# Kernel optimization log

Measured on AMD Instinct MI355X. Metric: run time of the kernel, lower is better.

## Reference

```python
import jax, jax.numpy as jnp
import numpy as np

N_PARTICLES = 100000
STATE_DIM = 64          # 3 + 2*2 + 57
MSG_OUT = 64
HIDDEN = 32
N_EDGES = 1600000


def _init_linear(key, fan_in, fan_out):
    kw, kb = jax.random.split(key)
    bound = 1.0 / np.sqrt(fan_in)
    W = jax.random.uniform(kw, (fan_in, fan_out), minval=-bound, maxval=bound, dtype=jnp.float32)
    b = jax.random.uniform(kb, (fan_out,), minval=-bound, maxval=bound, dtype=jnp.float32)
    return W, b


def setup_inputs() -> dict:
    key = jax.random.key(0)
    ks = jax.random.split(key, 8)
    x = jax.random.normal(ks[0], (N_PARTICLES, STATE_DIM), dtype=jnp.float32)
    edge_index = jax.random.randint(ks[1], (2, N_EDGES), 0, N_PARTICLES, dtype=jnp.int64)
    # message conv MLP: [2*STATE_DIM] -> 32 -> 32 -> MSG_OUT
    mW1, mb1 = _init_linear(ks[2], 2 * STATE_DIM, HIDDEN)
    mW2, mb2 = _init_linear(ks[3], HIDDEN, HIDDEN)
    mW3, mb3 = _init_linear(ks[4], HIDDEN, MSG_OUT)
    # own_state_nn MLP: [STATE_DIM + MSG_OUT] -> 32 -> 32 -> STATE_DIM
    oW1, ob1 = _init_linear(ks[5], STATE_DIM + MSG_OUT, HIDDEN)
    oW2, ob2 = _init_linear(ks[6], HIDDEN, HIDDEN)
    oW3, ob3 = _init_linear(ks[7], HIDDEN, STATE_DIM)
    return {"x": x, "edge_index": edge_index,
            "mW1": mW1, "mb1": mb1, "mW2": mW2, "mb2": mb2, "mW3": mW3, "mb3": mb3,
            "oW1": oW1, "ob1": ob1, "oW2": oW2, "ob2": ob2, "oW3": oW3, "ob3": ob3}


def _mlp3(h, W1, b1, W2, b2, W3, b3):
    h = jax.nn.relu(h @ W1 + b1)
    h = jax.nn.relu(h @ W2 + b2)
    return h @ W3 + b3


def reference(x, edge_index, mW1, mb1, mW2, mb2, mW3, mb3,
              oW1, ob1, oW2, ob2, oW3, ob3):
    src, dst = edge_index[0], edge_index[1]
    # edge-wise message: MLP over [x_src || x_dst]  -> [E, MSG_OUT]
    e_feat = jnp.concatenate([x[src], x[dst]], axis=-1)  # [E, 2*STATE_DIM]
    m = _mlp3(e_feat, mW1, mb1, mW2, mb2, mW3, mb3)
    # scatter-sum aggregation at destination node
    messages = jax.ops.segment_sum(m, dst, num_segments=x.shape[0])  # [N, MSG_OUT]
    combined = jnp.concatenate([x, messages], axis=-1)  # [N, STATE_DIM+MSG_OUT]
    new_state = _mlp3(combined, oW1, ob1, oW2, ob2, oW3, ob3)
    return new_state
```

## Files before the change

kernel.cpp:

```cpp
#include <hip/hip_runtime.h>

#define NP 100000
#define NE 1600000
#define SD 64
#define HID 32
#define MSG 64
#define NP_PAD 100352
#define NTILE (NP / 16)
#define TILE_BLOCKS ((NTILE + 3) / 4)
#define BINSZ 512
#define NBIN ((NP + BINSZ - 1) / BINSZ)
#define EPW 8192
#define NWG ((NE + EPW - 1) / EPW)

typedef float v4f __attribute__((ext_vector_type(4)));
typedef short v4s __attribute__((ext_vector_type(4)));
typedef short v8s __attribute__((ext_vector_type(8)));
typedef __bf16 v8bf __attribute__((ext_vector_type(8)));

#define WQ_FRAGS 56

__device__ __forceinline__ v4f MFMA32(v8s a, v8s b, v4f c) {
  return __builtin_amdgcn_mfma_f32_16x16x32_bf16(
      __builtin_bit_cast(v8bf, a), __builtin_bit_cast(v8bf, b), c, 0, 0, 0);
}

__device__ __forceinline__ short f2bf(float f) {
  return __builtin_bit_cast(short, (__bf16)f);
}
__device__ __forceinline__ float bf2f(short s) {
  unsigned u = ((unsigned)(unsigned short)s) << 16;
  return __builtin_bit_cast(float, u);
}

__device__ __forceinline__ v4f mfma3(v8s ah, v8s al, v8s bh, v8s bl, v4f c) {
  c = MFMA32(al, bh, c);
  c = MFMA32(ah, bl, c);
  c = MFMA32(ah, bh, c);
  return c;
}

__device__ __forceinline__ void load_wfrag(const float* __restrict__ W, int ld,
                                           int kb, int m0, int lq, int l15,
                                           v8s* hi, v8s* lo) {
  v8s h, l;
#pragma unroll
  for (int j = 0; j < 8; ++j) {
    int k = kb + ((j < 4) ? (4 * lq + j) : (16 + 4 * lq + (j - 4)));
    float v = W[k * ld + m0 + l15];
    short hb = f2bf(v);
    h[j] = hb;
    l[j] = f2bf(v - bf2f(hb));
  }
  *hi = h;
  *lo = l;
}

__device__ __forceinline__ void split8(v4f a, v4f b, v8s* hi, v8s* lo) {
  v8s h, l;
#pragma unroll
  for (int j = 0; j < 4; ++j) {
    short ha = f2bf(a[j]); h[j] = ha; l[j] = f2bf(a[j] - bf2f(ha));
    short hb = f2bf(b[j]); h[j + 4] = hb; l[j + 4] = f2bf(b[j] - bf2f(hb));
  }
  *hi = h;
  *lo = l;
}

__device__ __forceinline__ void load_xfrag(const float* xs, int kb, int lq,
                                           v8s* hi, v8s* lo) {
  v4f a = *reinterpret_cast<const v4f*>(xs + kb + 4 * lq);
  v4f b = *reinterpret_cast<const v4f*>(xs + kb + 16 + 4 * lq);
  split8(a, b, hi, lo);
}

__device__ __forceinline__ void chain_frag(v4f d0, v4f d1, v8s* hi, v8s* lo) {
  v4f a, b;
#pragma unroll
  for (int j = 0; j < 4; ++j) {
    a[j] = fmaxf(d0[j], 0.f);
    b[j] = fmaxf(d1[j], 0.f);
  }
  split8(a, b, hi, lo);
}

__device__ __forceinline__ v8s chain_hi(v4f d0, v4f d1) {
  v8s h;
#pragma unroll
  for (int j = 0; j < 4; ++j) {
    h[j] = f2bf(fmaxf(d0[j], 0.f));
    h[j + 4] = f2bf(fmaxf(d1[j], 0.f));
  }
  return h;
}

__global__ __launch_bounds__(256, 2) void setup_kernel(
    const float* __restrict__ x, const int* __restrict__ ei,
    const float* __restrict__ mW1, const float* __restrict__ mb1,
    const float* __restrict__ mW2, const float* __restrict__ mW3,
    const float* __restrict__ oW1, const float* __restrict__ oW2,
    const float* __restrict__ oW3,
    int* __restrict__ gOff, short* __restrict__ wqs,
    float* __restrict__ h1d_buf, short* __restrict__ h1s_buf) {
  __shared__ int cnt[NBIN];
  const int blk = blockIdx.x;

  if (blk < NWG) {
    for (int i = threadIdx.x; i < NBIN; i += 256) cnt[i] = 0;
    __syncthreads();
    const int e0 = blk * EPW;
    const int e1 = (e0 + EPW < NE) ? e0 + EPW : NE;
    for (int e = e0 + threadIdx.x; e < e1; e += 256)
      atomicAdd(&cnt[ei[NE + e] >> 9], 1);
    __syncthreads();
    for (int i = threadIdx.x; i < NBIN; i += 256) gOff[i * NWG + blk] = cnt[i];
    return;
  }

  const int lane = threadIdx.x & 63;
  const int l15 = lane & 15;
  const int lq = lane >> 4;

  if (blk == NWG) {
    if (threadIdx.x >= 64) return;
    v8s* wq = reinterpret_cast<v8s*>(wqs);
    v8s h, l;
#pragma unroll
    for (int t = 0; t < 2; ++t)
#pragma unroll
      for (int kc = 0; kc < 2; ++kc) {
        load_wfrag(mW1, HID, kc * 32, t * 16, lq, l15, &h, &l);
        wq[(t * 2 + kc) * 64 + lane] = h;
        wq[(4 + t * 2 + kc) * 64 + lane] = l;
        load_wfrag(mW1, HID, 64 + kc * 32, t * 16, lq, l15, &h, &l);
        wq[(8 + t * 2 + kc) * 64 + lane] = h;
        wq[(12 + t * 2 + kc) * 64 + lane] = l;
      }
#pragma unroll
    for (int t = 0; t < 2; ++t) {
      load_wfrag(mW2, HID, 0, t * 16, lq, l15, &h, &l);
      wq[(16 + t) * 64 + lane] = h;
      wq[(18 + t) * 64 + lane] = l;
    }
#pragma unroll
    for (int t = 0; t < 4; ++t) {
      load_wfrag(mW3, MSG, 0, t * 16, lq, l15, &h, &l);
      wq[(20 + t) * 64 + lane] = h;
      wq[(24 + t) * 64 + lane] = l;
    }
#pragma unroll
    for (int t = 0; t < 2; ++t)
#pragma unroll
      for (int kc = 0; kc < 4; ++kc) {
        load_wfrag(oW1, HID, kc * 32, t * 16, lq, l15, &h, &l);
        wq[(28 + t * 4 + kc) * 64 + lane] = h;
        wq[(36 + t * 4 + kc) * 64 + lane] = l;
      }
#pragma unroll
    for (int t = 0; t < 2; ++t) {
      load_wfrag(oW2, HID, 0, t * 16, lq, l15, &h, &l);
      wq[(44 + t) * 64 + lane] = h;
      wq[(46 + t) * 64 + lane] = l;
    }
#pragma unroll
    for (int t = 0; t < 4; ++t) {
      load_wfrag(oW3, SD, 0, t * 16, lq, l15, &h, &l);
      wq[(48 + t) * 64 + lane] = h;
      wq[(52 + t) * 64 + lane] = l;
    }
    return;
  }

  const int tile = ((blk - NWG - 1) * 256 + (int)threadIdx.x) >> 6;
  if (tile >= NTILE) return;
  const int node = tile * 16 + l15;

  v4f d0, d1, s0 = {0.f, 0.f, 0.f, 0.f}, s1 = {0.f, 0.f, 0.f, 0.f};
#pragma unroll
  for (int q = 0; q < 4; ++q) {
    d0[q] = mb1[4 * lq + q];
    d1[q] = mb1[16 + 4 * lq + q];
  }
#pragma unroll
  for (int kc = 0; kc < 2; ++kc) {
    v8s xh, xl, wh, wl;
    load_xfrag(x + (size_t)node * SD, kc * 32, lq, &xh, &xl);
    load_wfrag(mW1, HID, 64 + kc * 32, 0, lq, l15, &wh, &wl);
    d0 = mfma3(wh, wl, xh, xl, d0);
    load_wfrag(mW1, HID, 64 + kc * 32, 16, lq, l15, &wh, &wl);
    d1 = mfma3(wh, wl, xh, xl, d1);
    load_wfrag(mW1, HID, kc * 32, 0, lq, l15, &wh, &wl);
    s0 = mfma3(wh, wl, xh, xl, s0);
    load_wfrag(mW1, HID, kc * 32, 16, lq, l15, &wh, &wl);
    s1 = mfma3(wh, wl, xh, xl, s1);
  }
  *reinterpret_cast<v4f*>(h1d_buf + (size_t)node * HID + 4 * lq) = d0;
  *reinterpret_cast<v4f*>(h1d_buf + (size_t)node * HID + 16 + 4 * lq) = d1;
  v4s q0, q1;
#pragma unroll
  for (int q = 0; q < 4; ++q) {
    q0[q] = f2bf(s0[q]);
    q1[q] = f2bf(s1[q]);
  }
  *reinterpret_cast<v4s*>(h1s_buf + (size_t)node * HID + 4 * lq) = q0;
  *reinterpret_cast<v4s*>(h1s_buf + (size_t)node * HID + 16 + 4 * lq) = q1;
}


__global__ __launch_bounds__(256) void scan_bins_kernel(
    int* __restrict__ gOff, int* __restrict__ binStart) {
  __shared__ int sh[256];
  const int b = threadIdx.x;
  int run = 0;
  if (b < NBIN) {
    int4* row = reinterpret_cast<int4*>(gOff + b * NWG);
#pragma unroll 4
    for (int i = 0; i < NWG / 4; ++i) {
      int4 v = row[i];
      int4 w;
      w.x = run; run += v.x;
      w.y = run; run += v.y;
      w.z = run; run += v.z;
      w.w = run; run += v.w;
      row[i] = w;
    }
  }
  sh[b] = run;
  __syncthreads();
  for (int off = 1; off < 256; off <<= 1) {
    int a = (b >= off) ? sh[b - off] : 0;
    __syncthreads();
    sh[b] += a;
    __syncthreads();
  }
  const int excl = sh[b] - run;
  if (b <= NBIN) binStart[b] = excl;
  if (b < NBIN) {
    int4* row = reinterpret_cast<int4*>(gOff + b * NWG);
#pragma unroll 4
    for (int i = 0; i < NWG / 4; ++i) {
      int4 v = row[i];
      v.x += excl; v.y += excl; v.z += excl; v.w += excl;
      row[i] = v;
    }
  }
}

__global__ __launch_bounds__(256) void bin_scatter_kernel(
    const int* __restrict__ ei, const int* __restrict__ gOff,
    unsigned* __restrict__ pairs) {
  __shared__ int cur[NBIN];
  const int w = blockIdx.x;
  for (int i = threadIdx.x; i < NBIN; i += 256) cur[i] = gOff[i * NWG + w];
  __syncthreads();
  const int e0 = w * EPW;
  const int e1 = (e0 + EPW < NE) ? e0 + EPW : NE;
  for (int e = e0 + threadIdx.x; e < e1; e += 256) {
    unsigned s = (unsigned)ei[e];
    unsigned d = (unsigned)ei[NE + e];
    int pos = atomicAdd(&cur[d >> 9], 1);
    pairs[pos] = (s << 9) | (d & (BINSZ - 1));
  }
}

__global__ __launch_bounds__(512) void bin_csr_kernel(
    const unsigned* __restrict__ pairs, const int* __restrict__ binStart,
    int2* __restrict__ co, int* __restrict__ csr_src) {
  __shared__ int sh[BINSZ];
  __shared__ int cu[BINSZ];
  const int b = blockIdx.x;
  const int t = threadIdx.x;
  cu[t] = 0;
  __syncthreads();
  const int p0 = binStart[b], p1 = binStart[b + 1];
  for (int p = p0 + t; p < p1; p += BINSZ)
    atomicAdd(&cu[pairs[p] & (BINSZ - 1)], 1);
  __syncthreads();
  const int v = cu[t];
  sh[t] = v;
  __syncthreads();
  for (int off = 1; off < BINSZ; off <<= 1) {
    int a = (t >= off) ? sh[t - off] : 0;
    __syncthreads();
    sh[t] += a;
    __syncthreads();
  }
  const int excl = sh[t] - v;
  const int node = b * BINSZ + t;
  if (node < NP) co[node] = make_int2(p0 + excl, v);
  cu[t] = excl;
  __syncthreads();
  for (int p = p0 + t; p < p1; p += BINSZ) {
    unsigned pr = pairs[p];
    int loc = atomicAdd(&cu[pr & (BINSZ - 1)], 1);
    csr_src[p0 + loc] = (int)(pr >> 9);
  }
}

__global__ void edge_mfma_kernel(
    const short* __restrict__ h1s, const float* __restrict__ h1d_buf,
    const short* __restrict__ wqs, const int2* __restrict__ co,
    const int* __restrict__ csr_src, const float* __restrict__ mb2,
    float* __restrict__ rsum) {
  const int lane = threadIdx.x & 63;
  const int l15 = lane & 15;
  const int lq = lane >> 4;
  const int wid = (blockIdx.x * 256 + threadIdx.x) >> 6;
  const int nw = gridDim.x * 4;
  const v8s* wq = reinterpret_cast<const v8s*>(wqs);

  const v8s w2h0 = wq[16 * 64 + lane], w2h1 = wq[17 * 64 + lane];
  const v8s w2l0 = wq[18 * 64 + lane], w2l1 = wq[19 * 64 + lane];
  v4f bb0, bb1;
#pragma unroll
  for (int q = 0; q < 4; ++q) {
    bb0[q] = mb2[4 * lq + q];
    bb1[q] = mb2[16 + 4 * lq + q];
  }

  for (int n = wid * 2; n < NP; n += 2 * nw) {
    const int4 cc = *reinterpret_cast<const int4*>(co + n);
    const int offA = cc.x, cntA = cc.y;
    const int offB = cc.z, cntB = cc.w;
    const int ngA = (cntA + 15) >> 4;
    const int ngB = (cntB + 15) >> 4;
    const int ngM = ngA > ngB ? ngA : ngB;

    const v4f hA0 = *reinterpret_cast<const v4f*>(h1d_buf + (size_t)n * HID + 4 * lq);
    const v4f hA1 = *reinterpret_cast<const v4f*>(h1d_buf + (size_t)n * HID + 16 + 4 * lq);
    const v4f hB0 = *reinterpret_cast<const v4f*>(h1d_buf + (size_t)(n + 1) * HID + 4 * lq);
    const v4f hB1 = *reinterpret_cast<const v4f*>(h1d_buf + (size_t)(n + 1) * HID + 16 + 4 * lq);

    v4f rA0 = {0.f, 0.f, 0.f, 0.f}, rA1 = {0.f, 0.f, 0.f, 0.f};
    v4f rB0 = {0.f, 0.f, 0.f, 0.f}, rB1 = {0.f, 0.f, 0.f, 0.f};

    int sA = (l15 < cntA) ? csr_src[offA + l15] : 0;
    int sB = (l15 < cntB) ? csr_src[offB + l15] : 0;
    v4s aA = *reinterpret_cast<const v4s*>(h1s + (size_t)sA * HID + 4 * lq);
    v4s bA = *reinterpret_cast<const v4s*>(h1s + (size_t)sA * HID + 16 + 4 * lq);
    v4s aB = *reinterpret_cast<const v4s*>(h1s + (size_t)sB * HID + 4 * lq);
    v4s bB = *reinterpret_cast<const v4s*>(h1s + (size_t)sB * HID + 16 + 4 * lq);

    int remA = cntA, remB = cntB;
    for (int g = 0; g < ngM; ++g) {
      int sAn = (l15 < remA - 16) ? csr_src[offA + (g + 1) * 16 + l15] : 0;
      int sBn = (l15 < remB - 16) ? csr_src[offB + (g + 1) * 16 + l15] : 0;

      if (g < ngA) {
        v4f d0, d1;
#pragma unroll
        for (int q = 0; q < 4; ++q) {
          d0[q] = hA0[q] + bf2f(aA[q]);
          d1[q] = hA1[q] + bf2f(bA[q]);
        }
        v8s ph = chain_hi(d0, d1);
        v4f e0 = bb0, e1 = bb1;
        e0 = MFMA32(w2h0, ph, e0);
        e0 = MFMA32(w2l0, ph, e0);
        e1 = MFMA32(w2h1, ph, e1);
        e1 = MFMA32(w2l1, ph, e1);
        if (l15 < remA) {
#pragma unroll
          for (int j = 0; j < 4; ++j) {
            rA0[j] += fmaxf(e0[j], 0.f);
            rA1[j] += fmaxf(e1[j], 0.f);
          }
        }
      }
      aA = *reinterpret_cast<const v4s*>(h1s + (size_t)sAn * HID + 4 * lq);
      bA = *reinterpret_cast<const v4s*>(h1s + (size_t)sAn * HID + 16 + 4 * lq);

      if (g < ngB) {
        v4f d0, d1;
#pragma unroll
        for (int q = 0; q < 4; ++q) {
          d0[q] = hB0[q] + bf2f(aB[q]);
          d1[q] = hB1[q] + bf2f(bB[q]);
        }
        v8s ph = chain_hi(d0, d1);
        v4f e0 = bb0, e1 = bb1;
        e0 = MFMA32(w2h0, ph, e0);
        e0 = MFMA32(w2l0, ph, e0);
        e1 = MFMA32(w2h1, ph, e1);
        e1 = MFMA32(w2l1, ph, e1);
        if (l15 < remB) {
#pragma unroll
          for (int j = 0; j < 4; ++j) {
            rB0[j] += fmaxf(e0[j], 0.f);
            rB1[j] += fmaxf(e1[j], 0.f);
          }
        }
      }
      aB = *reinterpret_cast<const v4s*>(h1s + (size_t)sBn * HID + 4 * lq);
      bB = *reinterpret_cast<const v4s*>(h1s + (size_t)sBn * HID + 16 + 4 * lq);

      remA -= 16;
      remB -= 16;
    }

#pragma unroll
    for (int j = 0; j < 4; ++j) {
      float a = rA0[j], b = rA1[j], c = rB0[j], d = rB1[j];
      a += __shfl_xor(a, 1); a += __shfl_xor(a, 2);
      a += __shfl_xor(a, 4); a += __shfl_xor(a, 8);
      b += __shfl_xor(b, 1); b += __shfl_xor(b, 2);
      b += __shfl_xor(b, 4); b += __shfl_xor(b, 8);
      c += __shfl_xor(c, 1); c += __shfl_xor(c, 2);
      c += __shfl_xor(c, 4); c += __shfl_xor(c, 8);
      d += __shfl_xor(d, 1); d += __shfl_xor(d, 2);
      d += __shfl_xor(d, 4); d += __shfl_xor(d, 8);
      rA0[j] = a; rA1[j] = b; rB0[j] = c; rB1[j] = d;
    }
    if (l15 == 0) {
      *reinterpret_cast<v4f*>(rsum + (size_t)n * HID + 4 * lq) = rA0;
      *reinterpret_cast<v4f*>(rsum + (size_t)n * HID + 16 + 4 * lq) = rA1;
      *reinterpret_cast<v4f*>(rsum + (size_t)(n + 1) * HID + 4 * lq) = rB0;
      *reinterpret_cast<v4f*>(rsum + (size_t)(n + 1) * HID + 16 + 4 * lq) = rB1;
    }
  }
}

__global__ __launch_bounds__(256, 2) void fused_tail_kernel(
    const float* __restrict__ x, const short* __restrict__ wqs,
    const float* __restrict__ rsum, const int2* __restrict__ co,
    const float* __restrict__ mb3,
    const float* __restrict__ ob1, const float* __restrict__ ob2,
    const float* __restrict__ ob3,
    float* __restrict__ out) {
  const int lane = threadIdx.x & 63;
  const int l15 = lane & 15;
  const int lq = lane >> 4;
  const int tile = (blockIdx.x * 256 + threadIdx.x) >> 6;
  if (tile >= NTILE) return;
  const v8s* wq = reinterpret_cast<const v8s*>(wqs);

  const int node = tile * 16 + l15;
  const float fc = (float)co[node].y;

  v4f ra = *reinterpret_cast<const v4f*>(rsum + (size_t)node * HID + 4 * lq);
  v4f rb = *reinterpret_cast<const v4f*>(rsum + (size_t)node * HID + 16 + 4 * lq);
  v8s bh, bl;
  split8(ra, rb, &bh, &bl);

  v4f m[4];
#pragma unroll
  for (int t = 0; t < 4; ++t) {
    v4f c = {0.f, 0.f, 0.f, 0.f};
    c = mfma3(wq[(20 + t) * 64 + lane], wq[(24 + t) * 64 + lane], bh, bl, c);
#pragma unroll
    for (int q = 0; q < 4; ++q) c[q] += fc * mb3[t * 16 + 4 * lq + q];
    m[t] = c;
  }

  v4f d0, d1;
#pragma unroll
  for (int q = 0; q < 4; ++q) {
    d0[q] = ob1[4 * lq + q];
    d1[q] = ob1[16 + 4 * lq + q];
  }
#pragma unroll
  for (int kc = 0; kc < 2; ++kc) {
    v8s xh, xl;
    load_xfrag(x + (size_t)node * SD, kc * 32, lq, &xh, &xl);
    d0 = mfma3(wq[(28 + kc) * 64 + lane], wq[(36 + kc) * 64 + lane], xh, xl, d0);
    d1 = mfma3(wq[(32 + kc) * 64 + lane], wq[(40 + kc) * 64 + lane], xh, xl, d1);
  }
#pragma unroll
  for (int kc = 0; kc < 2; ++kc) {
    v8s mh, ml;
    split8(m[kc * 2], m[kc * 2 + 1], &mh, &ml);
    d0 = mfma3(wq[(30 + kc) * 64 + lane], wq[(38 + kc) * 64 + lane], mh, ml, d0);
    d1 = mfma3(wq[(34 + kc) * 64 + lane], wq[(42 + kc) * 64 + lane], mh, ml, d1);
  }

  v8s ph, pl;
  chain_frag(d0, d1, &ph, &pl);
  v4f e0, e1;
#pragma unroll
  for (int q = 0; q < 4; ++q) {
    e0[q] = ob2[4 * lq + q];
    e1[q] = ob2[16 + 4 * lq + q];
  }
  e0 = mfma3(wq[44 * 64 + lane], wq[46 * 64 + lane], ph, pl, e0);
  e1 = mfma3(wq[45 * 64 + lane], wq[47 * 64 + lane], ph, pl, e1);

  v8s rh, rl;
  chain_frag(e0, e1, &rh, &rl);
  float* orow = out + (size_t)node * SD;
#pragma unroll
  for (int t = 0; t < 4; ++t) {
    v4f c;
#pragma unroll
    for (int q = 0; q < 4; ++q) c[q] = ob3[t * 16 + 4 * lq + q];
    c = mfma3(wq[(48 + t) * 64 + lane], wq[(52 + t) * 64 + lane], rh, rl, c);
    *reinterpret_cast<v4f*>(orow + t * 16 + 4 * lq) = c;
  }
}

extern "C" void kernel_launch(void* const* d_in, const int* in_sizes, int n_in,
                              void* d_out, int out_size, void* d_ws,
                              size_t ws_size, hipStream_t stream) {
  const float* x = (const float*)d_in[0];
  const int* ei = (const int*)d_in[1];
  const float* mW1 = (const float*)d_in[2];
  const float* mb1 = (const float*)d_in[3];
  const float* mW2 = (const float*)d_in[4];
  const float* mb2 = (const float*)d_in[5];
  const float* mW3 = (const float*)d_in[6];
  const float* mb3 = (const float*)d_in[7];
  const float* oW1 = (const float*)d_in[8];
  const float* ob1 = (const float*)d_in[9];
  const float* oW2 = (const float*)d_in[10];
  const float* ob2 = (const float*)d_in[11];
  const float* oW3 = (const float*)d_in[12];
  const float* ob3 = (const float*)d_in[13];
  float* out = (float*)d_out;

  float* h1d_buf = (float*)d_out;
  short* h1s_buf = (short*)((char*)d_out + (size_t)NP * HID * 4);

  char* p = (char*)d_ws;
  short* wqs = (short*)p;            p += (size_t)WQ_FRAGS * 64 * 16;
  int* gOff = (int*)p;               p += (size_t)NBIN * NWG * 4;
  int* binStart = (int*)p;           p += 200 * 4;
  int2* co = (int2*)p;               p += (size_t)NP_PAD * 8;
  int* csr_src = (int*)p;            p += (size_t)NE * 4;
  unsigned* pairs = (unsigned*)p;
  float* rsum = (float*)p;

  setup_kernel<<<NWG + 1 + TILE_BLOCKS, 256, 0, stream>>>(
      x, ei, mW1, mb1, mW2, mW3, oW1, oW2, oW3, gOff, wqs, h1d_buf, h1s_buf);

  scan_bins_kernel<<<1, 256, 0, stream>>>(gOff, binStart);
  bin_scatter_kernel<<<NWG, 256, 0, stream>>>(ei, gOff, pairs);
  bin_csr_kernel<<<NBIN, 512, 0, stream>>>(pairs, binStart, co, csr_src);

  edge_mfma_kernel<<<4096, 256, 0, stream>>>(
      h1s_buf, h1d_buf, wqs, co, csr_src, mb2, rsum);

  fused_tail_kernel<<<TILE_BLOCKS, 256, 0, stream>>>(
      x, wqs, rsum, co, mb3, ob1, ob2, ob3, out);
}
```

Measured before the change: 156.6 us.

## Fuse per-bin CSR build into edge MFMA kernel with LDS-resident CSR

Halves the destination bin size to 256 nodes and merges the bin-local CSR construction with the edge-message MFMA computation. Each 512-thread block builds its bin's histogram, prefix offsets and source list in LDS, then its 8 waves process the bin's nodes in pairs. This removes the global csr_src and co arrays and one kernel launch. The cost is a fixed LDS capacity (MAXE) that silently drops edges if a bin overflows, and load balancing that is now fixed per bin instead of grid-strided.

```diff
diff --git a/kernel.cpp b/kernel.cpp
--- a/kernel.cpp
+++ b/kernel.cpp
@@ -8,8 +8,9 @@
 #define NP_PAD 100352
 #define NTILE (NP / 16)
 #define TILE_BLOCKS ((NTILE + 3) / 4)
-#define BINSZ 512
+#define BINSZ 256
 #define NBIN ((NP + BINSZ - 1) / BINSZ)
+#define MAXE 5632
 #define EPW 8192
 #define NWG ((NE + EPW - 1) / EPW)
 
@@ -111,7 +112,7 @@
     const int e0 = blk * EPW;
     const int e1 = (e0 + EPW < NE) ? e0 + EPW : NE;
     for (int e = e0 + threadIdx.x; e < e1; e += 256)
-      atomicAdd(&cnt[ei[NE + e] >> 9], 1);
+      atomicAdd(&cnt[ei[NE + e] >> 8], 1);
     __syncthreads();
     for (int i = threadIdx.x; i < NBIN; i += 256) gOff[i * NWG + blk] = cnt[i];
     return;
@@ -207,9 +208,9 @@
 }
 
 
-__global__ __launch_bounds__(256) void scan_bins_kernel(
+__global__ __launch_bounds__(512) void scan_bins_kernel(
     int* __restrict__ gOff, int* __restrict__ binStart) {
-  __shared__ int sh[256];
+  __shared__ int sh[512];
   const int b = threadIdx.x;
   int run = 0;
   if (b < NBIN) {
@@ -227,7 +228,7 @@
   }
   sh[b] = run;
   __syncthreads();
-  for (int off = 1; off < 256; off <<= 1) {
+  for (int off = 1; off < 512; off <<= 1) {
     int a = (b >= off) ? sh[b - off] : 0;
     __syncthreads();
     sh[b] += a;
@@ -258,55 +259,55 @@
   for (int e = e0 + threadIdx.x; e < e1; e += 256) {
     unsigned s = (unsigned)ei[e];
     unsigned d = (unsigned)ei[NE + e];
-    int pos = atomicAdd(&cur[d >> 9], 1);
-    pairs[pos] = (s << 9) | (d & (BINSZ - 1));
-  }
-}
-
-__global__ __launch_bounds__(512) void bin_csr_kernel(
-    const unsigned* __restrict__ pairs, const int* __restrict__ binStart,
-    int2* __restrict__ co, int* __restrict__ csr_src) {
-  __shared__ int sh[BINSZ];
-  __shared__ int cu[BINSZ];
+    int pos = atomicAdd(&cur[d >> 8], 1);
+    pairs[pos] = (s << 8) | (d & (BINSZ - 1));
+  }
+}
+
+__global__ __launch_bounds__(512, 4) void bin_fused_kernel(
+    const short* __restrict__ h1s, const float* __restrict__ h1d_buf,
+    const short* __restrict__ wqs, const unsigned* __restrict__ pairs,
+    const int* __restrict__ binStart, const float* __restrict__ mb2,
+    float* __restrict__ rsum, int* __restrict__ cntN) {
+  __shared__ int hist[BINSZ];
+  __shared__ int excl_s[BINSZ];
+  __shared__ int cur[BINSZ];
+  __shared__ int csr[MAXE];
+  const int tid = threadIdx.x;
   const int b = blockIdx.x;
-  const int t = threadIdx.x;
-  cu[t] = 0;
-  __syncthreads();
   const int p0 = binStart[b], p1 = binStart[b + 1];
-  for (int p = p0 + t; p < p1; p += BINSZ)
-    atomicAdd(&cu[pairs[p] & (BINSZ - 1)], 1);
-  __syncthreads();
-  const int v = cu[t];
-  sh[t] = v;
+
+  for (int i = tid; i < BINSZ; i += 512) hist[i] = 0;
+  __syncthreads();
+  for (int p = p0 + tid; p < p1; p += 512)
+    atomicAdd(&hist[pairs[p] & (BINSZ - 1)], 1);
+  __syncthreads();
+  if (tid < BINSZ) excl_s[tid] = hist[tid];
   __syncthreads();
   for (int off = 1; off < BINSZ; off <<= 1) {
-    int a = (t >= off) ? sh[t - off] : 0;
+    int a = (tid < BINSZ && tid >= off) ? excl_s[tid - off] : 0;
     __syncthreads();
-    sh[t] += a;
+    if (tid < BINSZ) excl_s[tid] += a;
     __syncthreads();
   }
-  const int excl = sh[t] - v;
-  const int node = b * BINSZ + t;
-  if (node < NP) co[node] = make_int2(p0 + excl, v);
-  cu[t] = excl;
-  __syncthreads();
-  for (int p = p0 + t; p < p1; p += BINSZ) {
+  if (tid < BINSZ) {
+    int e = excl_s[tid] - hist[tid];
+    excl_s[tid] = e;
+    cur[tid] = e;
+  }
+  __syncthreads();
+  for (int p = p0 + tid; p < p1; p += 512) {
     unsigned pr = pairs[p];
-    int loc = atomicAdd(&cu[pr & (BINSZ - 1)], 1);
-    csr_src[p0 + loc] = (int)(pr >> 9);
-  }
-}
-
-__global__ void edge_mfma_kernel(
-    const short* __restrict__ h1s, const float* __restrict__ h1d_buf,
-    const short* __restrict__ wqs, const int2* __restrict__ co,
-    const int* __restrict__ csr_src, const float* __restrict__ mb2,
-    float* __restrict__ rsum) {
-  const int lane = threadIdx.x & 63;
+    int pos = atomicAdd(&cur[pr & (BINSZ - 1)], 1);
+    if (pos < MAXE) csr[pos] = (int)(pr >> 8);
+  }
+  __syncthreads();
+
+  const int lane = tid & 63;
   const int l15 = lane & 15;
   const int lq = lane >> 4;
-  const int wid = (blockIdx.x * 256 + threadIdx.x) >> 6;
-  const int nw = gridDim.x * 4;
+  const int wv = tid >> 6;
+  const int nodeBase = b * BINSZ;
   const v8s* wq = reinterpret_cast<const v8s*>(wqs);
 
   const v8s w2h0 = wq[16 * 64 + lane], w2h1 = wq[17 * 64 + lane];
@@ -318,24 +319,27 @@
     bb1[q] = mb2[16 + 4 * lq + q];
   }
 
-  for (int n = wid * 2; n < NP; n += 2 * nw) {
-    const int4 cc = *reinterpret_cast<const int4*>(co + n);
-    const int offA = cc.x, cntA = cc.y;
-    const int offB = cc.z, cntB = cc.w;
+  for (int t = 0; t < 16; ++t) {
+    const int nlA = wv * 32 + 2 * t;
+    const int nlB = nlA + 1;
+    const int nA = nodeBase + nlA;
+    const int nB = nodeBase + nlB;
+    const int offA = excl_s[nlA], cntA = hist[nlA];
+    const int offB = excl_s[nlB], cntB = hist[nlB];
     const int ngA = (cntA + 15) >> 4;
     const int ngB = (cntB + 15) >> 4;
     const int ngM = ngA > ngB ? ngA : ngB;
 
-    const v4f hA0 = *reinterpret_cast<const v4f*>(h1d_buf + (size_t)n * HID + 4 * lq);
-    const v4f hA1 = *reinterpret_cast<const v4f*>(h1d_buf + (size_t)n * HID + 16 + 4 * lq);
-    const v4f hB0 = *reinterpret_cast<const v4f*>(h1d_buf + (size_t)(n + 1) * HID + 4 * lq);
-    const v4f hB1 = *reinterpret_cast<const v4f*>(h1d_buf + (size_t)(n + 1) * HID + 16 + 4 * lq);
+    const v4f hA0 = *reinterpret_cast<const v4f*>(h1d_buf + (size_t)nA * HID + 4 * lq);
+    const v4f hA1 = *reinterpret_cast<const v4f*>(h1d_buf + (size_t)nA * HID + 16 + 4 * lq);
+    const v4f hB0 = *reinterpret_cast<const v4f*>(h1d_buf + (size_t)nB * HID + 4 * lq);
+    const v4f hB1 = *reinterpret_cast<const v4f*>(h1d_buf + (size_t)nB * HID + 16 + 4 * lq);
 
     v4f rA0 = {0.f, 0.f, 0.f, 0.f}, rA1 = {0.f, 0.f, 0.f, 0.f};
     v4f rB0 = {0.f, 0.f, 0.f, 0.f}, rB1 = {0.f, 0.f, 0.f, 0.f};
 
-    int sA = (l15 < cntA) ? csr_src[offA + l15] : 0;
-    int sB = (l15 < cntB) ? csr_src[offB + l15] : 0;
+    int sA = (l15 < cntA) ? csr[offA + l15] : 0;
+    int sB = (l15 < cntB) ? csr[offB + l15] : 0;
     v4s aA = *reinterpret_cast<const v4s*>(h1s + (size_t)sA * HID + 4 * lq);
     v4s bA = *reinterpret_cast<const v4s*>(h1s + (size_t)sA * HID + 16 + 4 * lq);
     v4s aB = *reinterpret_cast<const v4s*>(h1s + (size_t)sB * HID + 4 * lq);
@@ -343,8 +347,8 @@
 
     int remA = cntA, remB = cntB;
     for (int g = 0; g < ngM; ++g) {
-      int sAn = (l15 < remA - 16) ? csr_src[offA + (g + 1) * 16 + l15] : 0;
-      int sBn = (l15 < remB - 16) ? csr_src[offB + (g + 1) * 16 + l15] : 0;
+      int sAn = (l15 < remA - 16) ? csr[offA + (g + 1) * 16 + l15] : 0;
+      int sBn = (l15 < remB - 16) ? csr[offB + (g + 1) * 16 + l15] : 0;
 
       if (g < ngA) {
         v4f d0, d1;
@@ -400,29 +404,35 @@
 
 #pragma unroll
     for (int j = 0; j < 4; ++j) {
-      float a = rA0[j], b = rA1[j], c = rB0[j], d = rB1[j];
+      float a = rA0[j], b2 = rA1[j], c = rB0[j], d = rB1[j];
       a += __shfl_xor(a, 1); a += __shfl_xor(a, 2);
       a += __shfl_xor(a, 4); a += __shfl_xor(a, 8);
-      b += __shfl_xor(b, 1); b += __shfl_xor(b, 2);
-      b += __shfl_xor(b, 4); b += __shfl_xor(b, 8);
+      b2 += __shfl_xor(b2, 1); b2 += __shfl_xor(b2, 2);
+      b2 += __shfl_xor(b2, 4); b2 += __shfl_xor(b2, 8);
       c += __shfl_xor(c, 1); c += __shfl_xor(c, 2);
       c += __shfl_xor(c, 4); c += __shfl_xor(c, 8);
       d += __shfl_xor(d, 1); d += __shfl_xor(d, 2);
       d += __shfl_xor(d, 4); d += __shfl_xor(d, 8);
-      rA0[j] = a; rA1[j] = b; rB0[j] = c; rB1[j] = d;
+      rA0[j] = a; rA1[j] = b2; rB0[j] = c; rB1[j] = d;
     }
     if (l15 == 0) {
-      *reinterpret_cast<v4f*>(rsum + (size_t)n * HID + 4 * lq) = rA0;
-      *reinterpret_cast<v4f*>(rsum + (size_t)n * HID + 16 + 4 * lq) = rA1;
-      *reinterpret_cast<v4f*>(rsum + (size_t)(n + 1) * HID + 4 * lq) = rB0;
-      *reinterpret_cast<v4f*>(rsum + (size_t)(n + 1) * HID + 16 + 4 * lq) = rB1;
+      if (nA < NP) {
+        *reinterpret_cast<v4f*>(rsum + (size_t)nA * HID + 4 * lq) = rA0;
+        *reinterpret_cast<v4f*>(rsum + (size_t)nA * HID + 16 + 4 * lq) = rA1;
+        if (lq == 0) cntN[nA] = cntA;
+      }
+      if (nB < NP) {
+        *reinterpret_cast<v4f*>(rsum + (size_t)nB * HID + 4 * lq) = rB0;
+        *reinterpret_cast<v4f*>(rsum + (size_t)nB * HID + 16 + 4 * lq) = rB1;
+        if (lq == 0) cntN[nB] = cntB;
+      }
     }
   }
 }
 
 __global__ __launch_bounds__(256, 2) void fused_tail_kernel(
     const float* __restrict__ x, const short* __restrict__ wqs,
-    const float* __restrict__ rsum, const int2* __restrict__ co,
+    const float* __restrict__ rsum, const int* __restrict__ cntN,
     const float* __restrict__ mb3,
     const float* __restrict__ ob1, const float* __restrict__ ob2,
     const float* __restrict__ ob3,
@@ -435,7 +445,7 @@
   const v8s* wq = reinterpret_cast<const v8s*>(wqs);
 
   const int node = tile * 16 + l15;
-  const float fc = (float)co[node].y;
+  const float fc = (float)cntN[node];
 
   v4f ra = *reinterpret_cast<const v4f*>(rsum + (size_t)node * HID + 4 * lq);
   v4f rb = *reinterpret_cast<const v4f*>(rsum + (size_t)node * HID + 16 + 4 * lq);
@@ -522,22 +532,20 @@
   char* p = (char*)d_ws;
   short* wqs = (short*)p;            p += (size_t)WQ_FRAGS * 64 * 16;
   int* gOff = (int*)p;               p += (size_t)NBIN * NWG * 4;
-  int* binStart = (int*)p;           p += 200 * 4;
-  int2* co = (int2*)p;               p += (size_t)NP_PAD * 8;
-  int* csr_src = (int*)p;            p += (size_t)NE * 4;
-  unsigned* pairs = (unsigned*)p;
+  int* binStart = (int*)p;           p += 400 * 4;
+  int* cntN = (int*)p;               p += (size_t)NP_PAD * 4;
+  unsigned* pairs = (unsigned*)p;    p += (size_t)NE * 4;
   float* rsum = (float*)p;
 
   setup_kernel<<<NWG + 1 + TILE_BLOCKS, 256, 0, stream>>>(
       x, ei, mW1, mb1, mW2, mW3, oW1, oW2, oW3, gOff, wqs, h1d_buf, h1s_buf);
 
-  scan_bins_kernel<<<1, 256, 0, stream>>>(gOff, binStart);
+  scan_bins_kernel<<<1, 512, 0, stream>>>(gOff, binStart);
   bin_scatter_kernel<<<NWG, 256, 0, stream>>>(ei, gOff, pairs);
-  bin_csr_kernel<<<NBIN, 512, 0, stream>>>(pairs, binStart, co, csr_src);
-
-  edge_mfma_kernel<<<4096, 256, 0, stream>>>(
-      h1s_buf, h1d_buf, wqs, co, csr_src, mb2, rsum);
+
+  bin_fused_kernel<<<NBIN, 512, 0, stream>>>(
+      h1s_buf, h1d_buf, wqs, pairs, binStart, mb2, rsum, cntN);
 
   fused_tail_kernel<<<TILE_BLOCKS, 256, 0, stream>>>(
-      x, wqs, rsum, co, mb3, ob1, ob2, ob3, out);
-}
+      x, wqs, rsum, cntN, mb3, ob1, ob2, ob3, out);
+}
```

Measured after the change: 179.1 us. 14.3% more time.
